# Performance work log

Measured on AMD Instinct MI355X. Metric: run time of the kernel, lower is better.

The kernel has to match this reference:

```python
import jax, jax.numpy as jnp
import numpy as np

INFTY_APPROX = 1e+30
ROTARY_BASE = 10000.0
D_HEAD = 128


def rope(x):
    # x: [B, H, T, D]
    *_, length, width = x.shape
    half = width // 2
    positions = jnp.arange(length)[:, None].astype(x.dtype)          # [T, 1]
    dims = jnp.arange(half).astype(x.dtype)                           # [half]
    ang_freqs = jnp.power(ROTARY_BASE, -dims / half)[None, :]         # [1, half]
    radians = positions * ang_freqs                                   # [T, half]
    cos = jnp.cos(radians)[None, None].astype(x.dtype)                # [1,1,T,half]
    sin = jnp.sin(radians)[None, None].astype(x.dtype)
    even, odd = jnp.split(x, 2, axis=-1)
    r_even = even * cos - odd * sin
    r_odd = even * sin + odd * cos
    return jnp.concatenate([r_even, r_odd], axis=-1)


def setup_inputs() -> dict:
    key = jax.random.key(0)
    ks = jax.random.split(key, 5)
    B, T, M, D = 4, 2048, 1024, D_HEAD
    H = M // D
    x = jax.random.normal(ks[0], (B, T, M), dtype=jnp.float32)
    scale = M ** -0.5
    wq = jax.random.normal(ks[1], (H, M, D), dtype=jnp.float32) * scale
    wk = jax.random.normal(ks[2], (H, M, D), dtype=jnp.float32) * scale
    wv = jax.random.normal(ks[3], (H, M, D), dtype=jnp.float32) * scale
    wo = jax.random.normal(ks[4], (H, D, M), dtype=jnp.float32) * scale
    return {"x": x, "wq": wq, "wk": wk, "wv": wv, "wo": wo}


def reference(x, wq, wk, wv, wo):
    # x: [B, T, M]; w{q,k,v}: [H, M, D]; wo: [H, D, M]
    q = jnp.einsum('bim,hmd->bhid', x, wq)
    k = jnp.einsum('bim,hmd->bhid', x, wk)
    v = jnp.einsum('bim,hmd->bhid', x, wv)
    q = rope(q)
    k = rope(k)
    # NOTE: module scales BOTH q and k by d_head**-0.5 (mup-style 1/d overall)
    mult = jnp.asarray(D_HEAD ** -0.5, dtype=x.dtype)
    s = jnp.einsum('bhid,bhjd->bhij', q * mult, k * mult)
    T = s.shape[-1]
    i = jnp.arange(T)[:, None]
    j = jnp.arange(T)[None, :]
    mask = (i < j).astype(s.dtype)[None, None]  # future positions masked
    s = s - jnp.asarray(INFTY_APPROX, dtype=s.dtype) * mask
    p = jax.nn.softmax(s, axis=-1)
    o = jnp.einsum('bhij,bhjd->bhid', p, v)
    r = jnp.einsum('bhid,hdm->bim', o, wo)
    return r
```

## Files before the change

kernel.cpp:

```cpp
#include <hip/hip_runtime.h>
#include <math.h>


typedef unsigned short u16;
typedef __attribute__((ext_vector_type(8))) short short8;
typedef __attribute__((ext_vector_type(4))) float floatx4;

#define MFMA_B16(a, b, c) __builtin_amdgcn_mfma_f32_16x16x32_bf16((a), (b), (c), 0, 0, 0)

__device__ __forceinline__ void async_cp16(const void* g, void* l) {
  __builtin_amdgcn_global_load_lds(
      (const __attribute__((address_space(1))) unsigned int*)g,
      (__attribute__((address_space(3))) unsigned int*)l, 16, 0, 0);
}

__device__ __forceinline__ u16 f2bf(float f) {
  unsigned u = __float_as_uint(f);
  u += 0x7FFFu + ((u >> 16) & 1u);
  return (u16)(u >> 16);
}

__device__ __forceinline__ int swz8(int row, int chunk) { return ((chunk ^ (row & 7)) << 3); }


__global__ void conv_x(const float* __restrict__ xf, u16* __restrict__ xb) {
  int idx = (blockIdx.x * 256 + threadIdx.x) * 4;
  float4 v = *(const float4*)(xf + idx);
  ushort4 o = make_ushort4(f2bf(v.x), f2bf(v.y), f2bf(v.z), f2bf(v.w));
  *(ushort4*)(xb + idx) = o;
}

__global__ void prep_wqkv(const float* __restrict__ wq, const float* __restrict__ wk,
                          const float* __restrict__ wv, u16* __restrict__ wT) {
  __shared__ float tile[32][33];
  const float* src = (blockIdx.z == 0) ? wq : (blockIdx.z == 1) ? wk : wv;
  u16* dst = wT + (size_t)blockIdx.z * 1024 * 1024;
  int h = blockIdx.y >> 2, dt = blockIdx.y & 3;
  int m0 = blockIdx.x * 32, d0 = dt * 32;
  int tx = threadIdx.x, ty = threadIdx.y;
#pragma unroll
  for (int i = 0; i < 4; i++) {
    int r = ty + i * 8;
    tile[r][tx] = src[((size_t)h * 1024 + m0 + r) * 128 + d0 + tx];
  }
  __syncthreads();
#pragma unroll
  for (int i = 0; i < 4; i++) {
    int r = ty + i * 8;
    dst[((size_t)h * 128 + d0 + r) * 1024 + m0 + tx] = f2bf(tile[tx][r]);
  }
}

__global__ void prep_wo(const float* __restrict__ wo, u16* __restrict__ woT) {
  __shared__ float tile[32][33];
  int r0 = blockIdx.y * 32, c0 = blockIdx.x * 32;
  int tx = threadIdx.x, ty = threadIdx.y;
#pragma unroll
  for (int i = 0; i < 4; i++) {
    int r = ty + i * 8;
    tile[r][tx] = wo[(size_t)(r0 + r) * 1024 + c0 + tx];
  }
  __syncthreads();
#pragma unroll
  for (int i = 0; i < 4; i++) {
    int r = ty + i * 8;
    woT[(size_t)(c0 + r) * 1024 + r0 + tx] = f2bf(tile[tx][r]);
  }
}

__global__ void prep_rope(float2* __restrict__ tab) {
  int idx = blockIdx.x * 256 + threadIdx.x;
  int t = idx >> 6, d = idx & 63;
  const float c1 = -0.20762050593046015f;
  float freq = exp2f((float)d * c1);
  float rad = (float)t * freq;
  float s, c;
  sincosf(rad, &s, &c);
  tab[idx] = make_float2(c, s);
}

template <int MODE>
__launch_bounds__(256, 2)
__global__ void gemm_bt(const u16* __restrict__ A, const u16* __restrict__ Bt,
                        void* __restrict__ out0, u16* __restrict__ out_k,
                        u16* __restrict__ out_v, const float2* __restrict__ ropetab) {
  __shared__ u16 smem[16384];
  u16* As = smem;
  u16* Bs = smem + 8192;
  const int tid = threadIdx.x;
  const int w = tid >> 6, lane = tid & 63, quad = lane >> 4, l15 = lane & 15;
  const int row0 = blockIdx.x * 128;
  const int by = blockIdx.y;
  const int n0 = by * 128;

  floatx4 acc[2][8] = {};

  for (int kt = 0; kt < 16; ++kt) {
    __syncthreads();
#pragma unroll
    for (int i = 0; i < 4; i++) {
      int cidx = (w * 4 + i) * 64 + lane;
      int r = cidx >> 3, c = cidx & 7, cg = c ^ (r & 7);
      async_cp16(A + (size_t)(row0 + r) * 1024 + kt * 64 + cg * 8, As + (w * 4 + i) * 512);
      async_cp16(Bt + (size_t)(n0 + r) * 1024 + kt * 64 + cg * 8, Bs + (w * 4 + i) * 512);
    }
    __syncthreads();
#pragma unroll
    for (int ks = 0; ks < 2; ks++) {
      short8 af[2];
#pragma unroll
      for (int mi = 0; mi < 2; mi++) {
        int r = w * 32 + mi * 16 + l15;
        af[mi] = *(const short8*)(As + r * 64 + swz8(r, ks * 4 + quad));
      }
#pragma unroll
      for (int ni = 0; ni < 8; ni++) {
        int n = ni * 16 + l15;
        short8 bf = *(const short8*)(Bs + n * 64 + swz8(n, ks * 4 + quad));
        acc[0][ni] = MFMA_B16(af[0], bf, acc[0][ni]);
        acc[1][ni] = MFMA_B16(af[1], bf, acc[1][ni]);
      }
    }
  }
  __syncthreads();

  if (MODE == 0) {
    int sel = by >> 3, h = by & 7;
    if (sel < 2) {
      u16* dst = sel ? out_k : (u16*)out0;
#pragma unroll
      for (int mi = 0; mi < 2; mi++) {
#pragma unroll
        for (int reg = 0; reg < 4; reg++) {
          int row = row0 + w * 32 + mi * 16 + quad * 4 + reg;
          int b = row >> 11, t = row & 2047;
          u16* drow = dst + ((size_t)(b * 8 + h) * 2048 + t) * 128;
#pragma unroll
          for (int ni = 0; ni < 4; ni++) {
            int d = ni * 16 + l15;
            float2 cs = ropetab[t * 64 + d];
            float e = acc[mi][ni][reg], o = acc[mi][ni + 4][reg];
            drow[d] = f2bf(e * cs.x - o * cs.y);
            drow[d + 64] = f2bf(e * cs.y + o * cs.x);
          }
        }
      }
    } else {
#pragma unroll
      for (int mi = 0; mi < 2; mi++) {
#pragma unroll
        for (int reg = 0; reg < 4; reg++) {
          int r = w * 32 + mi * 16 + quad * 4 + reg;
#pragma unroll
          for (int ni = 0; ni < 8; ni++) {
            int col = ni * 16 + l15;
            smem[r * 128 + swz8(r, col >> 3) + (col & 7)] = f2bf(acc[mi][ni][reg]);
          }
        }
      }
      __syncthreads();
      int tl = tid & 127, dg = tid >> 7;
      int row = row0 + tl;
      int b = row >> 11, t = row & 2047;
      u16* vdst = out_v + (size_t)(b * 8 + h) * 128 * 2048;
#pragma unroll
      for (int dd = 0; dd < 64; dd++) {
        int d = dg * 64 + dd;
        u16 val = smem[tl * 128 + swz8(tl, d >> 3) + (d & 7)];
        vdst[(size_t)d * 2048 + t] = val;
      }
    }
  } else {
    float* outf = (float*)out0;
#pragma unroll
    for (int mi = 0; mi < 2; mi++) {
#pragma unroll
      for (int reg = 0; reg < 4; reg++) {
        int row = row0 + w * 32 + mi * 16 + quad * 4 + reg;
#pragma unroll
        for (int ni = 0; ni < 8; ni++) {
          outf[(size_t)row * 1024 + n0 + ni * 16 + l15] = acc[mi][ni][reg];
        }
      }
    }
  }
}

__device__ __forceinline__ void stage_kv(const u16* kb, const u16* vb, int jt,
                                         u16* Kd, u16* Vd, int w, int lane) {
#pragma unroll
  for (int i = 0; i < 4; i++) {
    int cidx = (w * 4 + i) * 64 + lane;
    int rK = cidx >> 4, cK = cidx & 15, gK = cK ^ (rK & 7);
    async_cp16(kb + (size_t)(jt * 64 + rK) * 128 + gK * 8, Kd + (w * 4 + i) * 512);
    int rV = cidx >> 3, cV = cidx & 7, gV = cV ^ (rV & 7);
    async_cp16(vb + (size_t)rV * 2048 + jt * 64 + gV * 8, Vd + (w * 4 + i) * 512);
  }
}

__launch_bounds__(256, 4)
__global__ void flash_attn(const u16* __restrict__ Q, const u16* __restrict__ Kw,
                           const u16* __restrict__ Vw, u16* __restrict__ O) {
  __shared__ u16 Ks[64 * 128];
  __shared__ u16 Vs[128 * 64];
  __shared__ u16 Ps[64 * 64];
  const int tid = threadIdx.x;
  const int w = tid >> 6, lane = tid & 63, quad = lane >> 4, l15 = lane & 15;
  const int bh = blockIdx.y;
  const int qt = (int)((blockIdx.x + bh) & 31);
  const int i0 = qt * 64;
  const u16* qb = Q + (size_t)bh * 2048 * 128;
  const u16* kb = Kw + (size_t)bh * 2048 * 128;
  const u16* vb = Vw + (size_t)bh * 128 * 2048;
  const int b = bh >> 3, h = bh & 7;
  const float SC = 0.011271055f;

  short8 qf[4];
  {
    int qrow = i0 + w * 16 + l15;
#pragma unroll
    for (int ks = 0; ks < 4; ks++)
      qf[ks] = *(const short8*)(qb + (size_t)qrow * 128 + ks * 32 + quad * 8);
  }

  floatx4 accO[8] = {};
  float lrow[4] = {0.f, 0.f, 0.f, 0.f};

  stage_kv(kb, vb, 0, Ks, Vs, w, lane);

  for (int jt = 0; jt <= qt; ++jt) {
    __syncthreads();
    const bool diag = (jt == qt);

    floatx4 sa[4] = {};
#pragma unroll
    for (int jj = 0; jj < 4; jj++) {
      if (diag && jj > w) continue;
#pragma unroll
      for (int ks = 0; ks < 4; ks++) {
        int j = jj * 16 + l15;
        short8 bfr = *(const short8*)(Ks + j * 128 + swz8(j, ks * 4 + quad));
        sa[jj] = MFMA_B16(qf[ks], bfr, sa[jj]);
      }
    }

#pragma unroll
    for (int jj = 0; jj < 4; jj++) {
#pragma unroll
      for (int r = 0; r < 4; r++) {
        float s = sa[jj][r] * SC;
        if (diag) {
          int jg = jj * 16 + l15;
          int ig = w * 16 + quad * 4 + r;
          if (jg > ig) s = -1e30f;
        }
        float p = exp2f(s);
        lrow[r] += p;
        int pr = w * 16 + quad * 4 + r;
        int col = jj * 16 + l15;
        Ps[pr * 64 + swz8(pr, col >> 3) + (col & 7)] = f2bf(p);
      }
    }

#pragma unroll
    for (int k2 = 0; k2 < 2; k2++) {
      int prow = w * 16 + l15;
      short8 pa = *(const short8*)(Ps + prow * 64 + swz8(prow, k2 * 4 + quad));
#pragma unroll
      for (int nt = 0; nt < 8; nt++) {
        int dr = nt * 16 + l15;
        short8 vf = *(const short8*)(Vs + dr * 64 + swz8(dr, k2 * 4 + quad));
        accO[nt] = MFMA_B16(pa, vf, accO[nt]);
      }
    }

    __syncthreads();
    if (jt < qt) stage_kv(kb, vb, jt + 1, Ks, Vs, w, lane);
  }

#pragma unroll
  for (int off = 1; off < 16; off <<= 1)
#pragma unroll
    for (int r = 0; r < 4; r++) lrow[r] += __shfl_xor(lrow[r], off);

#pragma unroll
  for (int nt = 0; nt < 8; nt++) {
#pragma unroll
    for (int r = 0; r < 4; r++) {
      int t = i0 + w * 16 + quad * 4 + r;
      float ov = accO[nt][r] / fmaxf(lrow[r], 1e-30f);
      O[(((size_t)b * 2048 + t) * 8 + h) * 128 + nt * 16 + l15] = f2bf(ov);
    }
  }
}

extern "C" void kernel_launch(void* const* d_in, const int* in_sizes, int n_in,
                              void* d_out, int out_size, void* d_ws, size_t ws_size,
                              hipStream_t stream) {
  const float* x = (const float*)d_in[0];
  const float* wq = (const float*)d_in[1];
  const float* wk = (const float*)d_in[2];
  const float* wv = (const float*)d_in[3];
  const float* wo = (const float*)d_in[4];
  float* out = (float*)d_out;

  char* ws = (char*)d_ws;
  const size_t SZ = 16777216;
  u16* x_bf = (u16*)(ws);
  u16* q_ws = (u16*)(ws + SZ);
  u16* k_ws = (u16*)(ws + 2 * SZ);
  u16* v_ws = (u16*)(ws + 3 * SZ);
  u16* o_ws = (u16*)(ws + 4 * SZ);
  u16* wT = (u16*)(ws + 5 * SZ);
  u16* woT = (u16*)(ws + 5 * SZ + 6291456);
  float2* tab = (float2*)(ws + 5 * SZ + 6291456 + 2097152);

  conv_x<<<8192, 256, 0, stream>>>(x, x_bf);
  prep_wqkv<<<dim3(32, 32, 3), dim3(32, 8), 0, stream>>>(wq, wk, wv, wT);
  prep_wo<<<dim3(32, 32), dim3(32, 8), 0, stream>>>(wo, woT);
  prep_rope<<<512, 256, 0, stream>>>(tab);
  gemm_bt<0><<<dim3(64, 24), 256, 0, stream>>>(x_bf, wT, q_ws, k_ws, v_ws, tab);
  flash_attn<<<dim3(32, 32), 256, 0, stream>>>(q_ws, k_ws, v_ws, o_ws);
  gemm_bt<1><<<dim3(64, 8), 256, 0, stream>>>(o_ws, woT, out, nullptr, nullptr, nullptr);
}
```

Baseline: 258.7 us.

## Use 128-row query tiles with double-buffered K/V staging in flash attention

Each block of the attention kernel now handles 128 query rows instead of 64, with every wave computing two 16-row sub-tiles. Each K/V fragment read from LDS therefore feeds twice as many MFMAs, and K/V is loaded from global memory half as often. K/V tiles are double-buffered so the next tile's async load is issued before the current tile's compute, which removes one barrier per iteration. The tile ordering is mirrored across heads to balance causal work. The costs are more registers and LDS per block (launch bounds drop to 2 blocks per SM), half as many blocks, and waves sitting idle on fully masked tiles.

After: 285.8 us. +10.5%, slower.

```diff
diff --git a/kernel.cpp b/kernel.cpp
--- a/kernel.cpp
+++ b/kernel.cpp
@@ -198,100 +198,122 @@
   }
 }
 
-__launch_bounds__(256, 4)
+__launch_bounds__(256, 2)
 __global__ void flash_attn(const u16* __restrict__ Q, const u16* __restrict__ Kw,
                            const u16* __restrict__ Vw, u16* __restrict__ O) {
-  __shared__ u16 Ks[64 * 128];
-  __shared__ u16 Vs[128 * 64];
-  __shared__ u16 Ps[64 * 64];
+  __shared__ u16 smem[40960];
   const int tid = threadIdx.x;
   const int w = tid >> 6, lane = tid & 63, quad = lane >> 4, l15 = lane & 15;
   const int bh = blockIdx.y;
-  const int qt = (int)((blockIdx.x + bh) & 31);
-  const int i0 = qt * 64;
+  const int base = (int)((blockIdx.x + bh) & 15);
+  const int qt = (bh & 16) ? (15 - base) : base;
+  const int i0 = qt * 128;
+  const int njt = 2 * qt + 2;
   const u16* qb = Q + (size_t)bh * 2048 * 128;
   const u16* kb = Kw + (size_t)bh * 2048 * 128;
   const u16* vb = Vw + (size_t)bh * 128 * 2048;
   const int b = bh >> 3, h = bh & 7;
   const float SC = 0.011271055f;
-
-  short8 qf[4];
-  {
-    int qrow = i0 + w * 16 + l15;
+  u16* Ps = smem + 32768;
+
+  short8 qf[2][4];
+#pragma unroll
+  for (int mi = 0; mi < 2; mi++) {
+    int qrow = i0 + w * 32 + mi * 16 + l15;
 #pragma unroll
     for (int ks = 0; ks < 4; ks++)
-      qf[ks] = *(const short8*)(qb + (size_t)qrow * 128 + ks * 32 + quad * 8);
-  }
-
-  floatx4 accO[8] = {};
-  float lrow[4] = {0.f, 0.f, 0.f, 0.f};
-
-  stage_kv(kb, vb, 0, Ks, Vs, w, lane);
-
-  for (int jt = 0; jt <= qt; ++jt) {
+      qf[mi][ks] = *(const short8*)(qb + (size_t)qrow * 128 + ks * 32 + quad * 8);
+  }
+
+  floatx4 accO[2][8] = {};
+  float lrow[2][4] = {};
+
+  stage_kv(kb, vb, 0, smem, smem + 16384, w, lane);
+
+  for (int jt = 0; jt < njt; ++jt) {
     __syncthreads();
-    const bool diag = (jt == qt);
-
-    floatx4 sa[4] = {};
+    if (jt + 1 < njt)
+      stage_kv(kb, vb, jt + 1, smem + ((jt + 1) & 1) * 8192,
+               smem + 16384 + ((jt + 1) & 1) * 8192, w, lane);
+    const u16* Ks = smem + (jt & 1) * 8192;
+    const u16* Vs = smem + 16384 + (jt & 1) * 8192;
+
+    if ((jt * 64) > (i0 + w * 32 + 31)) continue;
+
+    const bool diag = (jt >= 2 * qt);
+    const int jrel0 = (jt - 2 * qt) * 64;
+
+    floatx4 sa[2][4] = {};
 #pragma unroll
     for (int jj = 0; jj < 4; jj++) {
-      if (diag && jj > w) continue;
 #pragma unroll
       for (int ks = 0; ks < 4; ks++) {
         int j = jj * 16 + l15;
         short8 bfr = *(const short8*)(Ks + j * 128 + swz8(j, ks * 4 + quad));
-        sa[jj] = MFMA_B16(qf[ks], bfr, sa[jj]);
-      }
-    }
-
-#pragma unroll
-    for (int jj = 0; jj < 4; jj++) {
-#pragma unroll
-      for (int r = 0; r < 4; r++) {
-        float s = sa[jj][r] * SC;
-        if (diag) {
-          int jg = jj * 16 + l15;
-          int ig = w * 16 + quad * 4 + r;
-          if (jg > ig) s = -1e30f;
-        }
-        float p = exp2f(s);
-        lrow[r] += p;
-        int pr = w * 16 + quad * 4 + r;
-        int col = jj * 16 + l15;
-        Ps[pr * 64 + swz8(pr, col >> 3) + (col & 7)] = f2bf(p);
+#pragma unroll
+        for (int mi = 0; mi < 2; mi++) {
+          if (!diag || (jrel0 + jj * 16 <= w * 32 + mi * 16 + 15))
+            sa[mi][jj] = MFMA_B16(qf[mi][ks], bfr, sa[mi][jj]);
+        }
+      }
+    }
+
+#pragma unroll
+    for (int mi = 0; mi < 2; mi++) {
+#pragma unroll
+      for (int jj = 0; jj < 4; jj++) {
+#pragma unroll
+        for (int r = 0; r < 4; r++) {
+          float s = sa[mi][jj][r] * SC;
+          if (diag) {
+            int jr = jrel0 + jj * 16 + l15;
+            int ir = w * 32 + mi * 16 + quad * 4 + r;
+            if (jr > ir) s = -1e30f;
+          }
+          float p = exp2f(s);
+          lrow[mi][r] += p;
+          int pr = w * 32 + mi * 16 + quad * 4 + r;
+          int col = jj * 16 + l15;
+          Ps[pr * 64 + swz8(pr, col >> 3) + (col & 7)] = f2bf(p);
+        }
       }
     }
 
 #pragma unroll
     for (int k2 = 0; k2 < 2; k2++) {
-      int prow = w * 16 + l15;
-      short8 pa = *(const short8*)(Ps + prow * 64 + swz8(prow, k2 * 4 + quad));
+      short8 pa[2];
+#pragma unroll
+      for (int mi = 0; mi < 2; mi++) {
+        int prow = w * 32 + mi * 16 + l15;
+        pa[mi] = *(const short8*)(Ps + prow * 64 + swz8(prow, k2 * 4 + quad));
+      }
 #pragma unroll
       for (int nt = 0; nt < 8; nt++) {
         int dr = nt * 16 + l15;
         short8 vf = *(const short8*)(Vs + dr * 64 + swz8(dr, k2 * 4 + quad));
-        accO[nt] = MFMA_B16(pa, vf, accO[nt]);
-      }
-    }
-
-    __syncthreads();
-    if (jt < qt) stage_kv(kb, vb, jt + 1, Ks, Vs, w, lane);
+        accO[0][nt] = MFMA_B16(pa[0], vf, accO[0][nt]);
+        accO[1][nt] = MFMA_B16(pa[1], vf, accO[1][nt]);
+      }
+    }
   }
 
 #pragma unroll
   for (int off = 1; off < 16; off <<= 1)
 #pragma unroll
-    for (int r = 0; r < 4; r++) lrow[r] += __shfl_xor(lrow[r], off);
-
-#pragma unroll
-  for (int nt = 0; nt < 8; nt++) {
-#pragma unroll
-    for (int r = 0; r < 4; r++) {
-      int t = i0 + w * 16 + quad * 4 + r;
-      float ov = accO[nt][r] / fmaxf(lrow[r], 1e-30f);
-      O[(((size_t)b * 2048 + t) * 8 + h) * 128 + nt * 16 + l15] = f2bf(ov);
-    }
-  }
+    for (int mi = 0; mi < 2; mi++)
+#pragma unroll
+      for (int r = 0; r < 4; r++) lrow[mi][r] += __shfl_xor(lrow[mi][r], off);
+
+#pragma unroll
+  for (int mi = 0; mi < 2; mi++)
+#pragma unroll
+    for (int nt = 0; nt < 8; nt++)
+#pragma unroll
+      for (int r = 0; r < 4; r++) {
+        int t = i0 + w * 32 + mi * 16 + quad * 4 + r;
+        float ov = accO[mi][nt][r] / fmaxf(lrow[mi][r], 1e-30f);
+        O[(((size_t)b * 2048 + t) * 8 + h) * 128 + nt * 16 + l15] = f2bf(ov);
+      }
 }
 
 extern "C" void kernel_launch(void* const* d_in, const int* in_sizes, int n_in,
@@ -320,6 +342,6 @@
   prep_wo<<<dim3(32, 32), dim3(32, 8), 0, stream>>>(wo, woT);
   prep_rope<<<512, 256, 0, stream>>>(tab);
   gemm_bt<0><<<dim3(64, 24), 256, 0, stream>>>(x_bf, wT, q_ws, k_ws, v_ws, tab);
-  flash_attn<<<dim3(32, 32), 256, 0, stream>>>(q_ws, k_ws, v_ws, o_ws);
+  flash_attn<<<dim3(16, 32), 256, 0, stream>>>(q_ws, k_ws, v_ws, o_ws);
   gemm_bt<1><<<dim3(64, 8), 256, 0, stream>>>(o_ws, woT, out, nullptr, nullptr, nullptr);
 }
```

## Keep P in registers by computing S transposed and using 16x16x16 MFMA for PV

Applied to the files above, without the earlier changes.

The QK^T MFMA now swaps its operands so each lane holds a column of S^T. That layout matches the A-operand layout of a 16x16x16 bf16 MFMA, so the probabilities feed the PV product straight from registers instead of going through a shared-memory P buffer. This removes the LDS writes and reads of P and its shared allocation, and adds diagonal-tile skipping in the PV loop. The trade-offs are twice as many PV MFMA instructions, each on half-width operands, narrower V loads, and a row-sum reduction done with lane shuffles.

After: 259.3 us. Within noise of the previous version (+0.2%).

```diff
diff --git a/kernel.cpp b/kernel.cpp
--- a/kernel.cpp
+++ b/kernel.cpp
@@ -4,9 +4,23 @@
 
 typedef unsigned short u16;
 typedef __attribute__((ext_vector_type(8))) short short8;
+typedef __attribute__((ext_vector_type(4))) short short4v;
 typedef __attribute__((ext_vector_type(4))) float floatx4;
 
 #define MFMA_B16(a, b, c) __builtin_amdgcn_mfma_f32_16x16x32_bf16((a), (b), (c), 0, 0, 0)
+
+__device__ __forceinline__ floatx4 mfma_16x16x16(short4v a, short4v b, floatx4 c) {
+#if __has_builtin(__builtin_amdgcn_mfma_f32_16x16x16bf16_1k)
+  return __builtin_amdgcn_mfma_f32_16x16x16bf16_1k(a, b, c, 0, 0, 0);
+#elif __has_builtin(__builtin_amdgcn_mfma_f32_16x16x16_bf16)
+  return __builtin_amdgcn_mfma_f32_16x16x16_bf16(a, b, c, 0, 0, 0);
+#else
+  floatx4 d;
+  asm volatile("v_mfma_f32_16x16x16_bf16 %0, %1, %2, %3"
+               : "=v"(d) : "v"(a), "v"(b), "v"(c));
+  return d;
+#endif
+}
 
 __device__ __forceinline__ void async_cp16(const void* g, void* l) {
   __builtin_amdgcn_global_load_lds(
@@ -203,7 +217,6 @@
                            const u16* __restrict__ Vw, u16* __restrict__ O) {
   __shared__ u16 Ks[64 * 128];
   __shared__ u16 Vs[128 * 64];
-  __shared__ u16 Ps[64 * 64];
   const int tid = threadIdx.x;
   const int w = tid >> 6, lane = tid & 63, quad = lane >> 4, l15 = lane & 15;
   const int bh = blockIdx.y;
@@ -224,7 +237,7 @@
   }
 
   floatx4 accO[8] = {};
-  float lrow[4] = {0.f, 0.f, 0.f, 0.f};
+  float lrow = 0.f;
 
   stage_kv(kb, vb, 0, Ks, Vs, w, lane);
 
@@ -239,38 +252,37 @@
 #pragma unroll
       for (int ks = 0; ks < 4; ks++) {
         int j = jj * 16 + l15;
-        short8 bfr = *(const short8*)(Ks + j * 128 + swz8(j, ks * 4 + quad));
-        sa[jj] = MFMA_B16(qf[ks], bfr, sa[jj]);
-      }
-    }
-
+        short8 kfr = *(const short8*)(Ks + j * 128 + swz8(j, ks * 4 + quad));
+        sa[jj] = MFMA_B16(kfr, qf[ks], sa[jj]);
+      }
+    }
+
+    short4v pfr[4];
 #pragma unroll
     for (int jj = 0; jj < 4; jj++) {
 #pragma unroll
       for (int r = 0; r < 4; r++) {
         float s = sa[jj][r] * SC;
         if (diag) {
-          int jg = jj * 16 + l15;
-          int ig = w * 16 + quad * 4 + r;
+          int jg = jj * 16 + quad * 4 + r;
+          int ig = w * 16 + l15;
           if (jg > ig) s = -1e30f;
         }
         float p = exp2f(s);
-        lrow[r] += p;
-        int pr = w * 16 + quad * 4 + r;
-        int col = jj * 16 + l15;
-        Ps[pr * 64 + swz8(pr, col >> 3) + (col & 7)] = f2bf(p);
-      }
-    }
-
-#pragma unroll
-    for (int k2 = 0; k2 < 2; k2++) {
-      int prow = w * 16 + l15;
-      short8 pa = *(const short8*)(Ps + prow * 64 + swz8(prow, k2 * 4 + quad));
+        lrow += p;
+        pfr[jj][r] = (short)f2bf(p);
+      }
+    }
+
+#pragma unroll
+    for (int jj = 0; jj < 4; jj++) {
+      if (diag && jj > w) continue;
 #pragma unroll
       for (int nt = 0; nt < 8; nt++) {
-        int dr = nt * 16 + l15;
-        short8 vf = *(const short8*)(Vs + dr * 64 + swz8(dr, k2 * 4 + quad));
-        accO[nt] = MFMA_B16(pa, vf, accO[nt]);
+        int d = nt * 16 + l15;
+        int j0 = jj * 16 + quad * 4;
+        short4v vfr = *(const short4v*)(Vs + d * 64 + (((j0 >> 3) ^ (d & 7)) << 3) + (j0 & 7));
+        accO[nt] = mfma_16x16x16(pfr[jj], vfr, accO[nt]);
       }
     }
 
@@ -278,17 +290,20 @@
     if (jt < qt) stage_kv(kb, vb, jt + 1, Ks, Vs, w, lane);
   }
 
-#pragma unroll
-  for (int off = 1; off < 16; off <<= 1)
-#pragma unroll
-    for (int r = 0; r < 4; r++) lrow[r] += __shfl_xor(lrow[r], off);
+  lrow += __shfl_xor(lrow, 16);
+  lrow += __shfl_xor(lrow, 32);
+
+  float linv[4];
+#pragma unroll
+  for (int r = 0; r < 4; r++)
+    linv[r] = 1.0f / fmaxf(__shfl(lrow, quad * 4 + r), 1e-30f);
 
 #pragma unroll
   for (int nt = 0; nt < 8; nt++) {
 #pragma unroll
     for (int r = 0; r < 4; r++) {
       int t = i0 + w * 16 + quad * 4 + r;
-      float ov = accO[nt][r] / fmaxf(lrow[r], 1e-30f);
+      float ov = accO[nt][r] * linv[r];
       O[(((size_t)b * 2048 + t) * 8 + h) * 128 + nt * 16 + l15] = f2bf(ov);
     }
   }
```
